# Kernel optimization log

Hardware: AMD Instinct MI355X
Metric: run time of the kernel (lower is better)

The kernel has to match this reference:

```python
import jax, jax.numpy as jnp
import numpy as np

B = 512; LH = 200; N = 40000; F = 256; E = 2000000; EF = 4
K = 8; LP = 50; P = 5000; D = 64; TD = 16; SK = 1000


def _time_enc(t):
    # TimeDualDecayEncoder stand-in: fixed log-spaced frequency cosine features (TGAT-style)
    freqs = 1.0 / (10.0 ** (jnp.arange(TD, dtype=jnp.float32) / TD * 5.0))
    return jnp.cos(t[..., None] * freqs)


def _layernorm(x, g, b):
    m = x.mean(-1, keepdims=True)
    v = ((x - m) ** 2).mean(-1, keepdims=True)
    return (x - m) * jax.lax.rsqrt(v + 1e-5) * g + b


def _gru(x, Wih, Whh, bih, bhh):
    # torch nn.GRU (batch_first), gate order r,z,n; returns final hidden state
    bsz, H = x.shape[0], Whh.shape[1]
    def step(h, xt):
        gi = xt @ Wih.T + bih
        gh = h @ Whh.T + bhh
        ir, iz, inn = jnp.split(gi, 3, -1)
        hr, hz, hn = jnp.split(gh, 3, -1)
        r = jax.nn.sigmoid(ir + hr)
        z = jax.nn.sigmoid(iz + hz)
        n = jnp.tanh(inn + r * hn)
        return (1.0 - z) * n + z * h, None
    h, _ = jax.lax.scan(step, jnp.zeros((bsz, H), x.dtype), jnp.swapaxes(x, 0, 1))
    return h


def _forward(src_node_ids, dst_node_ids, local_neighbor_ids, local_edge_ids, local_times,
             dst_neighbor_ids, dst_edge_ids, dst_times, retrieved_indices,
             node_raw, edge_raw, pool_nodes,
             Wfeat, bfeat, Wedge, bedge, Wtime, btime, Wstruct, bstruct, ln_g, ln_b,
             gruL_Wih, gruL_Whh, gruL_bih, gruL_bhh, gruQ_Wih, gruQ_Whh, gruQ_bih, gruQ_bhh,
             gcn_W, gcn_b, fus_W, fus_b, out_W, out_b):

    def dygkt(nids, eids, times, cur_dst, cur_skill):
        raw = node_raw[nids]                                   # (B,L,F) gather
        nf = raw @ Wfeat.T + bfeat
        ef = edge_raw[eids, 0:1] @ Wedge.T + bedge
        tf = _time_enc(times) @ Wtime.T + btime
        co = (nids == cur_dst[:, None]).astype(jnp.float32)[..., None]
        st = co @ Wstruct.T + bstruct
        sim = (raw[..., 0].astype(jnp.int32) == cur_skill[:, None]).astype(jnp.float32)[..., None]
        sk = sim @ Wstruct.T + bstruct
        return _layernorm(nf + ef + tf + st + sk, ln_g, ln_b)

    def graph_emb(demo):
        # demo: (K,LP) padded node-id sequences (0 = pad). Build dedup'd undirected
        # consecutive-pair graph, run GCNConv (self loops, sym norm), mean-pool.
        ids = demo.reshape(-1)
        M = ids.shape[0]
        valid = ids > 0
        sids = jnp.sort(jnp.where(valid, ids, N))               # invalid -> sentinel N
        uniq = (sids < N) & jnp.concatenate([jnp.ones((1,), bool), sids[1:] != sids[:-1]])
        x = node_raw[jnp.clip(sids, 0, N - 1)] @ Wfeat.T + bfeat
        h = (x @ gcn_W.T) * uniq[:, None]
        u = demo[:, :-1].reshape(-1)
        v = demo[:, 1:].reshape(-1)
        ve = (u > 0) & (v > 0)
        a = jnp.minimum(u, v); b = jnp.maximum(u, v)
        BIG = N * N                                             # fits int32 since N=40000
        skey = jnp.sort(jnp.where(ve, a * N + b, BIG))
        ew = ((skey < BIG) & jnp.concatenate([jnp.ones((1,), bool), skey[1:] != skey[:-1]])).astype(x.dtype)
        su = jnp.clip(jnp.searchsorted(sids, skey // N), 0, M - 1)
        sv = jnp.clip(jnp.searchsorted(sids, skey % N), 0, M - 1)
        uf = uniq.astype(x.dtype)
        deg = jnp.zeros(M, x.dtype).at[su].add(ew).at[sv].add(ew) + uf   # + self loop
        dis = jnp.where(deg > 0, jax.lax.rsqrt(deg), 0.0)
        nrm = (ew * dis[su] * dis[sv])[:, None]
        agg = jnp.zeros_like(h).at[sv].add(nrm * h[su]).at[su].add(nrm * h[sv])
        agg = agg + h * (dis * dis)[:, None] + gcn_b * uf[:, None]
        out = jax.nn.relu(agg)
        return out.sum(0) / jnp.maximum(uniq.sum(), 1).astype(x.dtype)

    dst_skill = node_raw[dst_node_ids, 0].astype(jnp.int32)
    src_skill = node_raw[src_node_ids, 0].astype(jnp.int32)
    local_emb = _gru(dygkt(local_neighbor_ids, local_edge_ids, local_times, dst_node_ids, dst_skill),
                     gruL_Wih, gruL_Whh, gruL_bih, gruL_bhh)
    glob = jax.vmap(graph_emb)(pool_nodes[retrieved_indices])   # (B,D)
    q_emb = _gru(dygkt(dst_neighbor_ids, dst_edge_ids, dst_times, src_node_ids, src_skill),
                 gruQ_Wih, gruQ_Whh, gruQ_bih, gruQ_bhh)
    fused = jax.nn.relu(jnp.concatenate([local_emb, glob], 1) @ fus_W.T + fus_b)
    return fused @ out_W.T + out_b, q_emb @ out_W.T + out_b


def setup_inputs() -> dict:
    key = jax.random.key(0)
    ks = jax.random.split(key, 32)
    f32 = jnp.float32
    node_raw = jax.random.normal(ks[0], (N, F), f32)
    node_raw = node_raw.at[:, 0].set(jax.random.randint(ks[1], (N,), 0, SK).astype(f32))
    edge_raw = jax.random.normal(ks[2], (E, EF), f32)
    ids = jax.random.randint(ks[3], (P, LP), 1, N)
    lens = jax.random.randint(ks[4], (P,), 2, LP + 1)
    pool_nodes = jnp.where(jnp.arange(LP)[None, :] < lens[:, None], ids, 0).astype(jnp.int32)
    def lin(k, o, i, s=0.05):
        kw, kb = jax.random.split(k)
        return jax.random.normal(kw, (o, i), f32) * s, jax.random.normal(kb, (o,), f32) * s
    Wfeat, bfeat = lin(ks[5], D, F)
    Wedge, bedge = lin(ks[6], D, 1)
    Wtime, btime = lin(ks[7], D, TD)
    Wstruct, bstruct = lin(ks[8], D, 1)
    gruL_Wih, gruL_bih = lin(ks[9], 3 * D, D)
    gruL_Whh, gruL_bhh = lin(ks[10], 3 * D, D)
    gruQ_Wih, gruQ_bih = lin(ks[11], 3 * D, D)
    gruQ_Whh, gruQ_bhh = lin(ks[12], 3 * D, D)
    gcn_W, gcn_b = lin(ks[13], D, D)
    fus_W, fus_b = lin(ks[14], D, 2 * D)
    out_W, out_b = lin(ks[15], D, D)
    return dict(
        src_node_ids=jax.random.randint(ks[16], (B,), 0, N).astype(jnp.int32),
        dst_node_ids=jax.random.randint(ks[17], (B,), 0, N).astype(jnp.int32),
        local_neighbor_ids=jax.random.randint(ks[18], (B, LH), 0, N).astype(jnp.int32),
        local_edge_ids=jax.random.randint(ks[19], (B, LH), 0, E).astype(jnp.int32),
        local_times=jax.random.uniform(ks[20], (B, LH), f32) * 100.0,
        dst_neighbor_ids=jax.random.randint(ks[21], (B, LH), 0, N).astype(jnp.int32),
        dst_edge_ids=jax.random.randint(ks[22], (B, LH), 0, E).astype(jnp.int32),
        dst_times=jax.random.uniform(ks[23], (B, LH), f32) * 100.0,
        retrieved_indices=jax.random.randint(ks[24], (B, K), 0, P).astype(jnp.int32),
        node_raw=node_raw, edge_raw=edge_raw, pool_nodes=pool_nodes,
        Wfeat=Wfeat, bfeat=bfeat, Wedge=Wedge, bedge=bedge, Wtime=Wtime, btime=btime,
        Wstruct=Wstruct, bstruct=bstruct, ln_g=jnp.ones((D,), f32), ln_b=jnp.zeros((D,), f32),
        gruL_Wih=gruL_Wih, gruL_Whh=gruL_Whh, gruL_bih=gruL_bih, gruL_bhh=gruL_bhh,
        gruQ_Wih=gruQ_Wih, gruQ_Whh=gruQ_Whh, gruQ_bih=gruQ_bih, gruQ_bhh=gruQ_bhh,
        gcn_W=gcn_W, gcn_b=gcn_b, fus_W=fus_W, fus_b=fus_b, out_W=out_W, out_b=out_b)


def reference(src_node_ids, dst_node_ids, local_neighbor_ids, local_edge_ids, local_times,
              dst_neighbor_ids, dst_edge_ids, dst_times, retrieved_indices,
              node_raw, edge_raw, pool_nodes,
              Wfeat, bfeat, Wedge, bedge, Wtime, btime, Wstruct, bstruct, ln_g, ln_b,
              gruL_Wih, gruL_Whh, gruL_bih, gruL_bhh, gruQ_Wih, gruQ_Whh, gruQ_bih, gruQ_bhh,
              gcn_W, gcn_b, fus_W, fus_b, out_W, out_b):
    return _forward(src_node_ids, dst_node_ids, local_neighbor_ids, local_edge_ids, local_times,
                    dst_neighbor_ids, dst_edge_ids, dst_times, retrieved_indices,
                    node_raw, edge_raw, pool_nodes,
                    Wfeat, bfeat, Wedge, bedge, Wtime, btime, Wstruct, bstruct, ln_g, ln_b,
                    gruL_Wih, gruL_Whh, gruL_bih, gruL_bhh, gruQ_Wih, gruQ_Whh, gruQ_bih, gruQ_bhh,
                    gcn_W, gcn_b, fus_W, fus_b, out_W, out_b)
```

## Files before the change

### kernel.cpp

```cpp
#include <hip/hip_runtime.h>
#include <math.h>

#define NN 40000
#define FF 256
#define DD 64
#define LHH 200
#define BB 512
#define TDD 16
#define GE_HASH 1024

typedef _Float16 h2f __attribute__((ext_vector_type(2)));

__constant__ float TFREQ[16] = {
    1.0f,            0.48696753f,    0.23713737f,    0.115478195f,
    0.056234132f,    0.027384196f,   0.013335215f,   0.0064938162f,
    0.0031622776f,   0.0015399265f,  0.00074989421f, 0.00036517414f,
    0.00017782794f,  8.6596433e-05f, 4.2169650e-05f, 2.0535251e-05f
};

__device__ __forceinline__ float fd2(unsigned a, unsigned b, float c) {
    union { unsigned u; h2f h; } ua, ub;
    ua.u = a; ub.u = b;
    return __builtin_amdgcn_fdot2(ua.h, ub.h, c, false);
}
__device__ __forceinline__ unsigned packrn(float a, float b) {
    union { h2f h; unsigned u; } x;
    x.h.x = (_Float16)a; x.h.y = (_Float16)b;
    return x.u;
}
__device__ __forceinline__ unsigned short f16u(float a) {
    union { _Float16 h; unsigned short u; } x;
    x.h = (_Float16)a;
    return x.u;
}
__device__ __forceinline__ float h16f(unsigned short u) {
    union { unsigned short u; _Float16 h; } x;
    x.u = u;
    return (float)x.h;
}
__device__ __forceinline__ float f16lo(unsigned u) {
    union { unsigned u; h2f h; } x; x.u = u; return (float)x.h.x;
}
__device__ __forceinline__ float f16hi(unsigned u) {
    union { unsigned u; h2f h; } x; x.u = u; return (float)x.h.y;
}
__device__ __forceinline__ unsigned pkrtz_u(float a, float b) {
    auto pk = __builtin_amdgcn_cvt_pkrtz(a, b);
    union { decltype(pk) h; unsigned u; } x;
    x.h = pk;
    return x.u;
}
__device__ __forceinline__ float dpp_xor1(float v) {
    return __int_as_float(
        __builtin_amdgcn_mov_dpp(__float_as_int(v), 0xB1, 0xF, 0xF, true));
}
__device__ __forceinline__ unsigned rlu(unsigned v, int l) {
    return (unsigned)__builtin_amdgcn_readlane((int)v, l);
}
__device__ __forceinline__ float sigm(float x) {
    return __builtin_amdgcn_rcpf(1.f + __expf(-x));
}
__device__ __forceinline__ float tanh_f(float x) {
    float e = __expf(2.f * x);
    return 1.f - 2.f * __builtin_amdgcn_rcpf(e + 1.f);
}
__device__ __forceinline__ int hlookupf(const unsigned* hkey, const int* hslot, unsigned id)
{
    unsigned p = (id * 2654435761u) & (GE_HASH - 1);
    while (hkey[p] != id) p = (p + 1) & (GE_HASH - 1);
    return hslot[p];
}

template<int KDIM>
__global__ void __launch_bounds__(256)
gemm_nt_kernel(const float* __restrict__ A, const float* __restrict__ W,
               const float* __restrict__ bias, float* __restrict__ C, int Nrows)
{
    __shared__ __align__(16) float a_t[128][8];
    __shared__ __align__(16) float wt[8][64];
    const int tid = threadIdx.x;
    const int tx = tid & 15;
    const int ty = tid >> 4;
    const int n0 = blockIdx.x * 128;

    float4 acc[8];
#pragma unroll
    for (int r = 0; r < 8; ++r) acc[r] = make_float4(0.f, 0.f, 0.f, 0.f);

    for (int kc = 0; kc < KDIM; kc += 8) {
        __syncthreads();
        {
            int r = tid >> 1;
            int cc = (tid & 1) * 4;
            int n = n0 + r;
            float4 v = make_float4(0.f, 0.f, 0.f, 0.f);
            if (n < Nrows) v = *(const float4*)(A + (size_t)n * KDIM + kc + cc);
            *(float4*)&a_t[r][cc] = v;
        }
        {
            int m = tid >> 2;
            int f0 = (tid & 3) * 2;
            float2 v = *(const float2*)(W + (size_t)m * KDIM + kc + f0);
            wt[f0][m] = v.x; wt[f0 + 1][m] = v.y;
        }
        __syncthreads();
        float4 w4[8];
#pragma unroll
        for (int f = 0; f < 8; ++f) w4[f] = *(float4*)&wt[f][tx * 4];
#pragma unroll
        for (int rr = 0; rr < 8; ++rr) {
            int row = ty + rr * 16;
            float4 a0 = *(float4*)&a_t[row][0];
            float4 a1 = *(float4*)&a_t[row][4];
            float av[8] = {a0.x, a0.y, a0.z, a0.w, a1.x, a1.y, a1.z, a1.w};
#pragma unroll
            for (int f = 0; f < 8; ++f) {
                acc[rr].x += av[f] * w4[f].x;
                acc[rr].y += av[f] * w4[f].y;
                acc[rr].z += av[f] * w4[f].z;
                acc[rr].w += av[f] * w4[f].w;
            }
        }
    }
    float4 bv = make_float4(0.f, 0.f, 0.f, 0.f);
    if (bias) bv = *(const float4*)(bias + tx * 4);
#pragma unroll
    for (int rr = 0; rr < 8; ++rr) {
        int n = n0 + ty + rr * 16;
        if (n < Nrows) {
            float4 o = acc[rr];
            o.x += bv.x; o.y += bv.y; o.z += bv.z; o.w += bv.w;
            *(float4*)(C + (size_t)n * DD + tx * 4) = o;
        }
    }
}

__global__ void __launch_bounds__(256)
tn_gemm_kernel(const float* __restrict__ proj,
               const float* __restrict__ WihL, const float* __restrict__ WihQ,
               const float* __restrict__ ln_g,
               unsigned short* __restrict__ TnL, unsigned short* __restrict__ TnQ)
{
    const float* Wih = blockIdx.y ? WihQ : WihL;
    unsigned short* Tn = blockIdx.y ? TnQ : TnL;
    __shared__ float wgT[64][193];
    __shared__ __align__(16) float4 at4[64][16];
    const int tid = threadIdx.x;
    const int n0 = blockIdx.x * 64;
    for (int i = tid; i < 192 * 64; i += 256) {
        int j = i >> 6, k = i & 63;
        wgT[k][j] = Wih[i] * ln_g[k];
    }
    for (int i = tid; i < 1024; i += 256) {
        int r = i >> 4, kc = i & 15;
        at4[r][kc] = ((const float4*)(proj + (size_t)(n0 + r) * DD))[kc];
    }
    __syncthreads();
    const int c = tid & 63, wv = tid >> 6;
    float acc0[16], acc1[16], acc2[16];
#pragma unroll
    for (int r = 0; r < 16; ++r) { acc0[r] = 0.f; acc1[r] = 0.f; acc2[r] = 0.f; }
    for (int kc = 0; kc < 16; ++kc) {
        float w0[4], w1[4], w2[4];
#pragma unroll
        for (int q = 0; q < 4; ++q) {
            w0[q] = wgT[kc * 4 + q][c];
            w1[q] = wgT[kc * 4 + q][64 + c];
            w2[q] = wgT[kc * 4 + q][128 + c];
        }
#pragma unroll
        for (int r = 0; r < 16; ++r) {
            float4 a = at4[wv * 16 + r][kc];
            acc0[r] += a.x * w0[0] + a.y * w0[1] + a.z * w0[2] + a.w * w0[3];
            acc1[r] += a.x * w1[0] + a.y * w1[1] + a.z * w1[2] + a.w * w1[3];
            acc2[r] += a.x * w2[0] + a.y * w2[1] + a.z * w2[2] + a.w * w2[3];
        }
    }
#pragma unroll
    for (int r = 0; r < 16; ++r) {
        size_t row = (size_t)(n0 + wv * 16 + r) * 192;
        Tn[row + c]       = f16u(acc0[r]);
        Tn[row + 64 + c]  = f16u(acc1[r]);
        Tn[row + 128 + c] = f16u(acc2[r]);
    }
}

__global__ void __launch_bounds__(192)
consts_kernel(const float* __restrict__ WihL, const float* __restrict__ bihL,
              const float* __restrict__ WhhL, float* __restrict__ outL,
              unsigned* __restrict__ whpL, unsigned* __restrict__ tpkL,
              const float* __restrict__ WihQ, const float* __restrict__ bihQ,
              const float* __restrict__ WhhQ, float* __restrict__ outQ,
              unsigned* __restrict__ whpQ, unsigned* __restrict__ tpkQ,
              unsigned* __restrict__ wtpk,
              const float* __restrict__ ln_g, const float* __restrict__ ln_b,
              const float* __restrict__ Wedge, const float* __restrict__ bedge,
              const float* __restrict__ Wtime, const float* __restrict__ btime,
              const float* __restrict__ Wstruct, const float* __restrict__ bstruct)
{
    const float* Wih = blockIdx.x ? WihQ : WihL;
    const float* bih = blockIdx.x ? bihQ : bihL;
    const float* Whh = blockIdx.x ? WhhQ : WhhL;
    float* out = blockIdx.x ? outQ : outL;
    unsigned* whp = blockIdx.x ? whpQ : whpL;
    unsigned* tpk = blockIdx.x ? tpkQ : tpkL;
    const int j = threadIdx.x;
    float te = 0.f, tw = 0.f, t1 = 0.f, tb0 = 0.f, cc = 0.f;
    float tt[16];
#pragma unroll
    for (int t = 0; t < 16; ++t) tt[t] = 0.f;
    for (int k = 0; k < DD; ++k) {
        float wv = Wih[j * DD + k];
        float wg = wv * ln_g[k];
        te  += wg * Wedge[k];
        tw  += wg * Wstruct[k];
        t1  += wg;
        tb0 += wg * (bedge[k] + btime[k] + 2.f * bstruct[k]);
        cc  += wv * ln_b[k];
#pragma unroll
        for (int t = 0; t < 16; ++t) tt[t] += wg * Wtime[k * TDD + t];
    }
    out[0 * 192 + j] = te;
    out[1 * 192 + j] = tw;
    out[2 * 192 + j] = t1;
    out[3 * 192 + j] = tb0;
    out[4 * 192 + j] = cc + bih[j];
    for (int t = 0; t < 16; ++t) out[(5 + t) * 192 + j] = tt[t];
    for (int q = 0; q < 8; ++q)
        tpk[j * 8 + q] = packrn(tt[2 * q], tt[2 * q + 1]);
    if (blockIdx.x == 0 && j < 64)
        for (int q = 0; q < 8; ++q)
            wtpk[j * 8 + q] = packrn(Wtime[j * TDD + 2 * q], Wtime[j * TDD + 2 * q + 1]);
    for (int k2 = 0; k2 < 32; ++k2)
        whp[j * 32 + k2] = packrn(Whh[j * DD + 2 * k2], Whh[j * DD + 2 * k2 + 1]);
}

struct PS {
    int nid;
    float tn0, tn1, tn2, pv, e0, sk, t;
};

__global__ void __launch_bounds__(256)
pre_kernel(const int* __restrict__ nidsL, const int* __restrict__ eidsL,
           const float* __restrict__ timesL, const int* __restrict__ curL,
           const int* __restrict__ nidsQ, const int* __restrict__ eidsQ,
           const float* __restrict__ timesQ, const int* __restrict__ curQ,
           const float* __restrict__ node_raw, const float* __restrict__ edge_raw,
           const float* __restrict__ proj_node,
           const unsigned short* __restrict__ TnL, const unsigned short* __restrict__ TnQ,
           const float* __restrict__ cstL, const float* __restrict__ cstQ,
           const unsigned* __restrict__ tpkL, const unsigned* __restrict__ tpkQ,
           const unsigned* __restrict__ wtpk,
           const float* __restrict__ bhhL, const float* __restrict__ bhhQ,
           const float* __restrict__ Wedge, const float* __restrict__ bedge,
           const float* __restrict__ Wtime, const float* __restrict__ btime,
           const float* __restrict__ Wstruct, const float* __restrict__ bstruct,
           unsigned* __restrict__ g01out, unsigned short* __restrict__ g2out)
{
    const int tid = threadIdx.x;
    const int d = tid & 63;
    const int seg = blockIdx.x * 4 + (tid >> 6);
    const int blk = seg >> 3, qq = seg & 7;
    const int g = blk >> 9, s = blk & 511;

    const int*            nids  = g ? nidsQ : nidsL;
    const int*            eids  = g ? eidsQ : eidsL;
    const float*          times = g ? timesQ : timesL;
    const int*            curp  = g ? curQ : curL;
    const unsigned short* Tn    = g ? TnQ : TnL;
    const float*          cst   = g ? cstQ : cstL;
    const unsigned*       tpk   = g ? tpkQ : tpkL;
    const float*          bhh   = g ? bhhQ : bhhL;

    unsigned tp0[8], tp1[8], tp2[8], wtp[8];
#pragma unroll
    for (int q4 = 0; q4 < 2; ++q4) {
        uint4 a = *(const uint4*)(tpk + (size_t)(0 * 64 + d) * 8 + 4 * q4);
        tp0[4*q4] = a.x; tp0[4*q4+1] = a.y; tp0[4*q4+2] = a.z; tp0[4*q4+3] = a.w;
        uint4 b = *(const uint4*)(tpk + (size_t)(1 * 64 + d) * 8 + 4 * q4);
        tp1[4*q4] = b.x; tp1[4*q4+1] = b.y; tp1[4*q4+2] = b.z; tp1[4*q4+3] = b.w;
        uint4 c = *(const uint4*)(tpk + (size_t)(2 * 64 + d) * 8 + 4 * q4);
        tp2[4*q4] = c.x; tp2[4*q4+1] = c.y; tp2[4*q4+2] = c.z; tp2[4*q4+3] = c.w;
        uint4 e = *(const uint4*)(wtpk + (size_t)d * 8 + 4 * q4);
        wtp[4*q4] = e.x; wtp[4*q4+1] = e.y; wtp[4*q4+2] = e.z; wtp[4*q4+3] = e.w;
    }
    const float TE0 = cst[0*192 + d], TE1 = cst[0*192 + 64 + d], TE2 = cst[0*192 + 128 + d];
    const float TW0 = cst[1*192 + d], TW1 = cst[1*192 + 64 + d], TW2 = cst[1*192 + 128 + d];
    const float T10 = cst[2*192 + d], T11 = cst[2*192 + 64 + d], T12 = cst[2*192 + 128 + d];
    const float TB0 = cst[3*192 + d], TB1 = cst[3*192 + 64 + d], TB2 = cst[3*192 + 128 + d];
    const float CC0 = cst[4*192 + d] + bhh[d];
    const float CC1 = cst[4*192 + 64 + d] + bhh[64 + d];
    const float CC2 = cst[4*192 + 128 + d];
    const float we_l = Wedge[d];
    const float ws_l = Wstruct[d];
    const float b0_l = bedge[d] + btime[d] + 2.f * bstruct[d];
    const float tfl  = TFREQ[d & 15];

    const int cur = curp[s];
    const int csk = (int)node_raw[(size_t)cur * FF];
    const int* nrow = nids + s * LHH;
    const int* erow = eids + s * LHH;
    const float* trow = times + s * LHH;
    const int lbase = qq * 25;

    auto GATH = [&](PS& P, int i) {
        int l = lbase + i;
        int nid = nrow[l];
        int eid = erow[l];
        P.nid = nid;
        const unsigned short* tb = Tn + (size_t)nid * 192;
        P.tn0 = h16f(tb[d]);
        P.tn1 = h16f(tb[64 + d]);
        P.tn2 = h16f(tb[128 + d]);
        P.pv  = proj_node[(size_t)nid * DD + d];
        P.e0  = edge_raw[(size_t)eid * 4];
        P.sk  = node_raw[(size_t)nid * FF];
        P.t   = trow[l];
    };

    auto EMIT = [&](const PS& P, int i) {
        float cv = __cosf(P.t * tfl);
        float cx = dpp_xor1(cv);
        unsigned cp = pkrtz_u(cv, cx);
        unsigned s0 = rlu(cp, 0),  s1 = rlu(cp, 2),  s2 = rlu(cp, 4),  s3 = rlu(cp, 6);
        unsigned s4 = rlu(cp, 8),  s5 = rlu(cp, 10), s6 = rlu(cp, 12), s7 = rlu(cp, 14);
        float tf = fd2(wtp[7], s7, fd2(wtp[6], s6, fd2(wtp[5], s5, fd2(wtp[4], s4, 0.f))));
        tf = fd2(wtp[3], s3, fd2(wtp[2], s2, fd2(wtp[1], s1, fd2(wtp[0], s0, tf))));
        float flg = ((P.nid == cur) ? 1.f : 0.f) + (((int)P.sk == csk) ? 1.f : 0.f);
        float f = P.pv + P.e0 * we_l + flg * ws_l + b0_l + tf;
        float mu = f;
#pragma unroll
        for (int off = 32; off; off >>= 1) mu += __shfl_xor(mu, off);
        mu *= (1.f / 64.f);
        float dv = f - mu, var = dv * dv;
#pragma unroll
        for (int off = 32; off; off >>= 1) var += __shfl_xor(var, off);
        float rs = rsqrtf(var * (1.f / 64.f) + 1e-5f);
        float c0 = fd2(tp0[7], s7, fd2(tp0[6], s6, fd2(tp0[5], s5, fd2(tp0[4], s4, 0.f))));
        c0 = fd2(tp0[3], s3, fd2(tp0[2], s2, fd2(tp0[1], s1, fd2(tp0[0], s0, c0))));
        float c1 = fd2(tp1[7], s7, fd2(tp1[6], s6, fd2(tp1[5], s5, fd2(tp1[4], s4, 0.f))));
        c1 = fd2(tp1[3], s3, fd2(tp1[2], s2, fd2(tp1[1], s1, fd2(tp1[0], s0, c1))));
        float c2 = fd2(tp2[7], s7, fd2(tp2[6], s6, fd2(tp2[5], s5, fd2(tp2[4], s4, 0.f))));
        c2 = fd2(tp2[3], s3, fd2(tp2[2], s2, fd2(tp2[1], s1, fd2(tp2[0], s0, c2))));
        float g0 = (c0 + P.tn0 + P.e0 * TE0 + flg * TW0 + TB0 - mu * T10) * rs + CC0;
        float g1 = (c1 + P.tn1 + P.e0 * TE1 + flg * TW1 + TB1 - mu * T11) * rs + CC1;
        float g2 = (c2 + P.tn2 + P.e0 * TE2 + flg * TW2 + TB2 - mu * T12) * rs + CC2;
        size_t pos = ((size_t)blk * LHH + (lbase + i)) * 64 + d;
        g01out[pos] = packrn(g0, g1);
        g2out[pos] = f16u(g2);
    };

    PS A, B, C;
    GATH(A, 0);
    GATH(B, 1);
    for (int i = 0; i < 25; ++i) {
        int inext = (i + 2 < 25) ? i + 2 : 24;
        GATH(C, inext);
        EMIT(A, i);
        A = B; B = C;
    }
}

__global__ void __launch_bounds__(64) __attribute__((amdgpu_waves_per_eu(1, 1)))
gru_lite_kernel(const unsigned* __restrict__ g01, const unsigned short* __restrict__ g2a,
                const unsigned* __restrict__ whpL, const unsigned* __restrict__ whpQ,
                const float* __restrict__ bhhL, const float* __restrict__ bhhQ,
                float* __restrict__ embL, float* __restrict__ embQ)
{
    const int blk = blockIdx.x;
    const int g = blk >> 9, s = blk & 511;
    const int d = threadIdx.x;

    const unsigned* whp = g ? whpQ : whpL;
    const float*    bhh = g ? bhhQ : bhhL;
    float*          emb = g ? embQ : embL;

    unsigned w0[32], w1[32], w2[32];
    {
        const unsigned* p0 = whp + (size_t)d * 32;
        const unsigned* p1 = whp + (size_t)(64 + d) * 32;
        const unsigned* p2 = whp + (size_t)(128 + d) * 32;
#pragma unroll
        for (int q4 = 0; q4 < 8; ++q4) {
            uint4 a = *(const uint4*)(p0 + 4 * q4);
            w0[4*q4] = a.x; w0[4*q4+1] = a.y; w0[4*q4+2] = a.z; w0[4*q4+3] = a.w;
            uint4 b = *(const uint4*)(p1 + 4 * q4);
            w1[4*q4] = b.x; w1[4*q4+1] = b.y; w1[4*q4+2] = b.z; w1[4*q4+3] = b.w;
            uint4 c = *(const uint4*)(p2 + 4 * q4);
            w2[4*q4] = c.x; w2[4*q4+1] = c.y; w2[4*q4+2] = c.z; w2[4*q4+3] = c.w;
        }
    }
#pragma unroll
    for (int i = 0; i < 32; ++i) {
        asm volatile("" : "+v"(w0[i]));
        asm volatile("" : "+v"(w1[i]));
        asm volatile("" : "+v"(w2[i]));
    }
    const float BH2 = bhh[128 + d];

    const unsigned* p01 = g01 + (size_t)blk * LHH * 64 + d;
    const unsigned short* p2 = g2a + (size_t)blk * LHH * 64 + d;

    float h = 0.f;

    auto COMPUTE = [&](unsigned pk01, unsigned pk2) {
        float g0 = f16lo(pk01), g1 = f16hi(pk01);
        float g2 = h16f((unsigned short)pk2);
        float hx = dpp_xor1(h);
        unsigned hpu = pkrtz_u(h, hx);
        float a0 = 0.f, a1 = 0.f, a2 = 0.f, e0 = 0.f, e1 = 0.f, e2 = 0.f;
#pragma unroll
        for (int q = 0; q < 32; q += 2) {
            unsigned sa = rlu(hpu, 2 * q);
            unsigned sb = rlu(hpu, 2 * q + 2);
            a0 = fd2(w0[q], sa, a0);
            a1 = fd2(w1[q], sa, a1);
            a2 = fd2(w2[q], sa, a2);
            e0 = fd2(w0[q+1], sb, e0);
            e1 = fd2(w1[q+1], sb, e1);
            e2 = fd2(w2[q+1], sb, e2);
        }
        float mv0 = a0 + e0, mv1 = a1 + e1, mv2 = a2 + e2;
        float r = sigm(g0 + mv0);
        float z = sigm(g1 + mv1);
        float n = tanh_f(g2 + r * (mv2 + BH2));
        h = (1.f - z) * n + z * h;
    };

    unsigned A01[4], A2[4], B01[4], B2[4];
#pragma unroll
    for (int i = 0; i < 4; ++i) {
        A01[i] = p01[(size_t)i * 64];
        A2[i]  = p2[(size_t)i * 64];
    }
    for (int l = 0; l < LHH; l += 8) {
#pragma unroll
        for (int i = 0; i < 4; ++i) {
            int ll = l + 4 + i;
            B01[i] = p01[(size_t)ll * 64];
            B2[i]  = p2[(size_t)ll * 64];
        }
#pragma unroll
        for (int i = 0; i < 4; ++i) COMPUTE(A01[i], A2[i]);
#pragma unroll
        for (int i = 0; i < 4; ++i) {
            int ll = l + 8 + i;
            if (ll > LHH - 1) ll = LHH - 1;
            A01[i] = p01[(size_t)ll * 64];
            A2[i]  = p2[(size_t)ll * 64];
        }
#pragma unroll
        for (int i = 0; i < 4; ++i) COMPUTE(B01[i], B2[i]);
    }
    emb[(size_t)s * DD + d] = h;
}

__global__ void __launch_bounds__(512)
dedup_kernel(const int* __restrict__ retrieved, const int* __restrict__ pool_nodes,
             int* __restrict__ slot_idG, float* __restrict__ disG,
             unsigned* __restrict__ startG, unsigned short* __restrict__ adjG,
             int* __restrict__ Ub)
{
    __shared__ unsigned hkey[GE_HASH];
    __shared__ int hslot[GE_HASH];
    __shared__ unsigned ekey[GE_HASH];
    __shared__ int ids[400];
    __shared__ int slot_id[400];
    __shared__ unsigned deg[400];
    __shared__ float dis[400];
    __shared__ unsigned elist[400];
    __shared__ unsigned scanA[400], scanB[400];
    __shared__ int cursor[400];
    __shared__ unsigned short adjS[800];
    __shared__ int pids[8];
    __shared__ int cntU, cntE;

    const int b = blockIdx.x;
    const int tid = threadIdx.x;

    if (tid < 8) pids[tid] = retrieved[b * 8 + tid];
    if (tid == 0) { cntU = 0; cntE = 0; }
    for (int i = tid; i < GE_HASH; i += 512) { hkey[i] = 0u; ekey[i] = 0u; }
    if (tid < 400) deg[tid] = 0u;
    __syncthreads();

    if (tid < 400) {
        int k = tid / 50, p = tid % 50;
        ids[tid] = pool_nodes[(size_t)pids[k] * 50 + p];
    }
    __syncthreads();

    if (tid < 400) {
        int idi = ids[tid];
        if (idi > 0) {
            unsigned id = (unsigned)idi;
            unsigned p = (id * 2654435761u) & (GE_HASH - 1);
            while (true) {
                unsigned old = atomicCAS(&hkey[p], 0u, id);
                if (old == 0u) {
                    int s = atomicAdd(&cntU, 1);
                    hslot[p] = s; slot_id[s] = idi;
                    break;
                }
                if (old == id) break;
                p = (p + 1) & (GE_HASH - 1);
            }
        }
    }
    __syncthreads();

    if (tid < 8 * 49) {
        int k = tid / 49, p = tid % 49;
        int u = ids[k * 50 + p], v = ids[k * 50 + p + 1];
        if (u > 0 && v > 0) {
            unsigned a = (unsigned)min(u, v), bb = (unsigned)max(u, v);
            unsigned key = a * 40000u + bb;
            unsigned p2 = (key * 2654435761u) & (GE_HASH - 1);
            while (true) {
                unsigned old = atomicCAS(&ekey[p2], 0u, key);
                if (old == 0u) {
                    int su = hlookupf(hkey, hslot, a);
                    int sv = hlookupf(hkey, hslot, bb);
                    int e = atomicAdd(&cntE, 1);
                    elist[e] = ((unsigned)su << 16) | (unsigned)sv;
                    atomicAdd(&deg[su], 1u);
                    atomicAdd(&deg[sv], 1u);
                    break;
                }
                if (old == key) break;
                p2 = (p2 + 1) & (GE_HASH - 1);
            }
        }
    }
    __syncthreads();

    const int U = cntU, EC = cntE;
    if (tid < 400) {
        dis[tid] = rsqrtf((float)deg[tid] + 1.0f);
        scanA[tid] = deg[tid];
    }
    __syncthreads();

    unsigned* src = scanA;
    unsigned* dst = scanB;
    for (int off = 1; off < 400; off <<= 1) {
        if (tid < 400)
            dst[tid] = src[tid] + ((tid >= off) ? src[tid - off] : 0u);
        __syncthreads();
        unsigned* t = src; src = dst; dst = t;
    }
    if (tid < 400) {
        unsigned st = src[tid] - deg[tid];
        cursor[tid] = (int)st;
        if (tid < U) startG[(size_t)b * 404 + tid] = st;
    }
    if (tid == 0) {
        startG[(size_t)b * 404 + U] = (U > 0) ? src[U - 1] : 0u;
        Ub[b] = U;
    }
    __syncthreads();

    if (tid < EC) {
        unsigned pk = elist[tid];
        int su = (int)(pk >> 16), sv = (int)(pk & 0xffffu);
        int pu = atomicAdd(&cursor[su], 1);
        adjS[pu] = (unsigned short)sv;
        int pv = atomicAdd(&cursor[sv], 1);
        adjS[pv] = (unsigned short)su;
    }
    __syncthreads();

    if (tid < 400) {
        slot_idG[(size_t)b * 400 + tid] = (tid < U) ? slot_id[tid] : 0;
        disG[(size_t)b * 400 + tid] = dis[tid];
    }
    for (int i = tid; i < 800; i += 512) {
        unsigned tot = (U > 0) ? src[U - 1] : 0u;
        adjG[(size_t)b * 800 + i] = (i < (int)tot) ? adjS[i] : (unsigned short)0;
    }
}

__global__ void __launch_bounds__(256)
gcn_agg_kernel(const float* __restrict__ hgcn, const float* __restrict__ gcn_b,
               const int* __restrict__ slot_idG, const float* __restrict__ disG,
               const unsigned* __restrict__ startG, const unsigned short* __restrict__ adjG,
               const int* __restrict__ Ub, float* __restrict__ part)
{
    __shared__ int sidS[400];
    __shared__ float disS[400];
    __shared__ unsigned stS[404];
    __shared__ unsigned short adjS[800];
    __shared__ float red[4][64];

    const int b = blockIdx.x, q = blockIdx.y;
    const int tid = threadIdx.x;
    const int lane = tid & 63, w = tid >> 6;
    const int U = Ub[b];

    for (int i = tid; i < 400; i += 256) {
        sidS[i] = slot_idG[(size_t)b * 400 + i];
        disS[i] = disG[(size_t)b * 400 + i];
    }
    for (int i = tid; i < 404; i += 256) stS[i] = startG[(size_t)b * 404 + i];
    for (int i = tid; i < 800; i += 256) adjS[i] = adjG[(size_t)b * 800 + i];
    __syncthreads();

    const float gb = gcn_b[lane];
    float acc = 0.f;

    for (int s = q * 4 + w; s < U; s += 16) {
        int nid = sidS[s];
        float ds = disS[s];
        float v = fmaf(ds * ds, hgcn[(size_t)nid * 64 + lane], gb);
        int a0 = (int)stS[s];
        int cnt = (int)stS[s + 1] - a0;
        for (int e0 = 0; e0 < cnt; e0 += 4) {
            float hv[4], nr[4];
#pragma unroll
            for (int j = 0; j < 4; ++j) {
                int e = e0 + j;
                int ec = (e < cnt) ? e : cnt - 1;
                int o = adjS[a0 + ec];
                nr[j] = (e < cnt) ? ds * disS[o] : 0.f;
                hv[j] = hgcn[(size_t)sidS[o] * 64 + lane];
            }
            v += nr[0] * hv[0] + nr[1] * hv[1] + nr[2] * hv[2] + nr[3] * hv[3];
        }
        acc += fmaxf(v, 0.f);
    }

    red[w][lane] = acc;
    __syncthreads();
    if (tid < 64)
        part[((size_t)b * 4 + q) * 64 + tid] =
            red[0][tid] + red[1][tid] + red[2][tid] + red[3][tid];
}

__global__ void __launch_bounds__(64)
head_kernel(const float* __restrict__ local_emb, const float* __restrict__ part,
            const int* __restrict__ Ub, const float* __restrict__ q_emb,
            const float* __restrict__ fus_W, const float* __restrict__ fus_b,
            const float* __restrict__ out_W, const float* __restrict__ out_b,
            float* __restrict__ out)
{
    __shared__ float cat[128];
    __shared__ float fus[64];
    __shared__ float qv[64];
    const int b = blockIdx.x, d = threadIdx.x;
    cat[d] = local_emb[(size_t)b * 64 + d];
    {
        const float* pb = part + (size_t)b * 4 * 64;
        float gsum = pb[d] + pb[64 + d] + pb[128 + d] + pb[192 + d];
        cat[64 + d] = gsum / (float)max(Ub[b], 1);
    }
    qv[d] = q_emb[(size_t)b * 64 + d];
    __syncthreads();
    float acc = fus_b[d];
    const float* fw = fus_W + (size_t)d * 128;
#pragma unroll 4
    for (int k = 0; k < 128; ++k) acc += cat[k] * fw[k];
    fus[d] = fmaxf(acc, 0.f);
    __syncthreads();
    float o0 = out_b[d], o1 = out_b[d];
    const float* ow = out_W + (size_t)d * 64;
#pragma unroll 4
    for (int k = 0; k < 64; ++k) { float ww = ow[k]; o0 += fus[k] * ww; o1 += qv[k] * ww; }
    out[(size_t)b * 64 + d] = o0;
    out[(size_t)BB * 64 + (size_t)b * 64 + d] = o1;
}

extern "C" void kernel_launch(void* const* d_in, const int* in_sizes, int n_in,
                              void* d_out, int out_size, void* d_ws, size_t ws_size,
                              hipStream_t stream)
{
    const int*   src_ids    = (const int*)d_in[0];
    const int*   dst_ids    = (const int*)d_in[1];
    const int*   l_nids     = (const int*)d_in[2];
    const int*   l_eids     = (const int*)d_in[3];
    const float* l_times    = (const float*)d_in[4];
    const int*   d_nids     = (const int*)d_in[5];
    const int*   d_eids     = (const int*)d_in[6];
    const float* d_times    = (const float*)d_in[7];
    const int*   retr       = (const int*)d_in[8];
    const float* node_raw   = (const float*)d_in[9];
    const float* edge_raw   = (const float*)d_in[10];
    const int*   pool_nodes = (const int*)d_in[11];
    const float* Wfeat  = (const float*)d_in[12];
    const float* bfeat  = (const float*)d_in[13];
    const float* Wedge  = (const float*)d_in[14];
    const float* bedge  = (const float*)d_in[15];
    const float* Wtime  = (const float*)d_in[16];
    const float* btime  = (const float*)d_in[17];
    const float* Wstruct= (const float*)d_in[18];
    const float* bstruct= (const float*)d_in[19];
    const float* ln_g   = (const float*)d_in[20];
    const float* ln_b   = (const float*)d_in[21];
    const float* gruL_Wih = (const float*)d_in[22];
    const float* gruL_Whh = (const float*)d_in[23];
    const float* gruL_bih = (const float*)d_in[24];
    const float* gruL_bhh = (const float*)d_in[25];
    const float* gruQ_Wih = (const float*)d_in[26];
    const float* gruQ_Whh = (const float*)d_in[27];
    const float* gruQ_bih = (const float*)d_in[28];
    const float* gruQ_bhh = (const float*)d_in[29];
    const float* gcn_W  = (const float*)d_in[30];
    const float* gcn_b  = (const float*)d_in[31];
    const float* fus_W  = (const float*)d_in[32];
    const float* fus_b  = (const float*)d_in[33];
    const float* out_W  = (const float*)d_in[34];
    const float* out_b  = (const float*)d_in[35];

    char* wsb = (char*)d_ws;
    auto alloc = [&](size_t bytes) -> void* {
        void* p = (void*)wsb;
        wsb += (bytes + 255) & ~(size_t)255;
        return p;
    };
    float*          proj_node = (float*)alloc((size_t)NN * DD * 4);
    float*          hgcn      = (float*)alloc((size_t)NN * DD * 4);
    unsigned short* TnL16     = (unsigned short*)alloc((size_t)NN * 192 * 2);
    unsigned short* TnQ16     = (unsigned short*)alloc((size_t)NN * 192 * 2);
    float*          cstL      = (float*)alloc(4096 * 4);
    float*          cstQ      = (float*)alloc(4096 * 4);
    unsigned*       whpL      = (unsigned*)alloc(192 * 32 * 4);
    unsigned*       whpQ      = (unsigned*)alloc(192 * 32 * 4);
    unsigned*       tpkL      = (unsigned*)alloc(192 * 8 * 4);
    unsigned*       tpkQ      = (unsigned*)alloc(192 * 8 * 4);
    unsigned*       wtpk      = (unsigned*)alloc(64 * 8 * 4);
    unsigned*       g01       = (unsigned*)alloc((size_t)2 * BB * LHH * 64 * 4);
    unsigned short* g2a       = (unsigned short*)alloc((size_t)2 * BB * LHH * 64 * 2);
    int*            slot_idG  = (int*)alloc((size_t)BB * 400 * 4);
    float*          disG      = (float*)alloc((size_t)BB * 400 * 4);
    unsigned*       startG    = (unsigned*)alloc((size_t)BB * 404 * 4);
    unsigned short* adjG      = (unsigned short*)alloc((size_t)BB * 800 * 2);
    int*            Ubuf      = (int*)alloc((size_t)BB * 4);
    float*          part      = (float*)alloc((size_t)BB * 4 * 64 * 4);
    float*          local_emb = (float*)alloc((size_t)BB * DD * 4);
    float*          q_emb     = (float*)alloc((size_t)BB * DD * 4);

    dim3 g1((NN + 127) / 128);
    gemm_nt_kernel<FF><<<g1, 256, 0, stream>>>(node_raw, Wfeat, bfeat, proj_node, NN);

    consts_kernel<<<2, 192, 0, stream>>>(gruL_Wih, gruL_bih, gruL_Whh, cstL, whpL, tpkL,
                                         gruQ_Wih, gruQ_bih, gruQ_Whh, cstQ, whpQ, tpkQ,
                                         wtpk, ln_g, ln_b, Wedge, bedge, Wtime, btime,
                                         Wstruct, bstruct);

    tn_gemm_kernel<<<dim3(NN / 64, 2), 256, 0, stream>>>(proj_node, gruL_Wih, gruQ_Wih,
                                                         ln_g, TnL16, TnQ16);

    dedup_kernel<<<BB, 512, 0, stream>>>(retr, pool_nodes, slot_idG, disG,
                                         startG, adjG, Ubuf);

    pre_kernel<<<2 * BB * 2, 256, 0, stream>>>(
        l_nids, l_eids, l_times, dst_ids,
        d_nids, d_eids, d_times, src_ids,
        node_raw, edge_raw, proj_node, TnL16, TnQ16, cstL, cstQ,
        tpkL, tpkQ, wtpk, gruL_bhh, gruQ_bhh,
        Wedge, bedge, Wtime, btime, Wstruct, bstruct,
        g01, g2a);

    gemm_nt_kernel<DD><<<g1, 256, 0, stream>>>(proj_node, gcn_W, nullptr, hgcn, NN);

    gru_lite_kernel<<<2 * BB, 64, 0, stream>>>(
        g01, g2a, whpL, whpQ, gruL_bhh, gruQ_bhh, local_emb, q_emb);

    gcn_agg_kernel<<<dim3(BB, 4), 256, 0, stream>>>(
        hgcn, gcn_b, slot_idG, disG, startG, adjG, Ubuf, part);

    head_kernel<<<BB, 64, 0, stream>>>(local_emb, part, Ubuf, q_emb,
        fus_W, fus_b, out_W, out_b, (float*)d_out);
}
```

Before: 294.9 us.

## Compact gathered node/edge scalars and projections to fp16 before pre_kernel

Adds a compaction kernel that pulls the skill scalar out of node_raw and edge feature 0 out of edge_raw into dense fp16/u16 arrays. tn_gemm also writes an fp16 copy of proj_node. pre_kernel then gathers from these narrow arrays instead of doing strided fp32 row gathers, which cuts scattered memory traffic. The cost is a full strided pass over the 2M-edge table (about 32MB read) every call, plus fp16 rounding of the projection and edge features, and skill values truncated to 16 bits.

```diff
diff --git a/kernel.cpp b/kernel.cpp
--- a/kernel.cpp
+++ b/kernel.cpp
@@ -7,6 +7,7 @@
 #define LHH 200
 #define BB 512
 #define TDD 16
+#define EE 2000000
 #define GE_HASH 1024
 
 typedef _Float16 h2f __attribute__((ext_vector_type(2)));
@@ -69,6 +70,18 @@
     unsigned p = (id * 2654435761u) & (GE_HASH - 1);
     while (hkey[p] != id) p = (p + 1) & (GE_HASH - 1);
     return hslot[p];
+}
+
+__global__ void __launch_bounds__(256)
+compact_kernel(const float* __restrict__ node_raw, const float* __restrict__ edge_raw,
+               unsigned short* __restrict__ skill16, unsigned short* __restrict__ e016)
+{
+    const int stride = gridDim.x * 256;
+    int i = blockIdx.x * 256 + threadIdx.x;
+    for (int n = i; n < NN; n += stride)
+        skill16[n] = (unsigned short)(int)node_raw[(size_t)n * FF];
+    for (int e = i; e < EE; e += stride)
+        e016[e] = f16u(edge_raw[(size_t)e * 4]);
 }
 
 template<int KDIM>
@@ -139,7 +152,8 @@
 tn_gemm_kernel(const float* __restrict__ proj,
                const float* __restrict__ WihL, const float* __restrict__ WihQ,
                const float* __restrict__ ln_g,
-               unsigned short* __restrict__ TnL, unsigned short* __restrict__ TnQ)
+               unsigned short* __restrict__ TnL, unsigned short* __restrict__ TnQ,
+               unsigned short* __restrict__ proj16)
 {
     const float* Wih = blockIdx.y ? WihQ : WihL;
     unsigned short* Tn = blockIdx.y ? TnQ : TnL;
@@ -156,6 +170,11 @@
         at4[r][kc] = ((const float4*)(proj + (size_t)(n0 + r) * DD))[kc];
     }
     __syncthreads();
+    if (blockIdx.y == 0) {
+        const float* atf = (const float*)at4;
+        for (int i = tid; i < 64 * 64; i += 256)
+            proj16[(size_t)(n0 + (i >> 6)) * DD + (i & 63)] = f16u(atf[i]);
+    }
     const int c = tid & 63, wv = tid >> 6;
     float acc0[16], acc1[16], acc2[16];
 #pragma unroll
@@ -236,8 +255,8 @@
 }
 
 struct PS {
-    int nid;
-    float tn0, tn1, tn2, pv, e0, sk, t;
+    int nid, skI;
+    float tn0, tn1, tn2, pv, e0, t;
 };
 
 __global__ void __launch_bounds__(256)
@@ -245,8 +264,8 @@
            const float* __restrict__ timesL, const int* __restrict__ curL,
            const int* __restrict__ nidsQ, const int* __restrict__ eidsQ,
            const float* __restrict__ timesQ, const int* __restrict__ curQ,
-           const float* __restrict__ node_raw, const float* __restrict__ edge_raw,
-           const float* __restrict__ proj_node,
+           const unsigned short* __restrict__ skill16, const unsigned short* __restrict__ e016,
+           const unsigned short* __restrict__ proj16,
            const unsigned short* __restrict__ TnL, const unsigned short* __restrict__ TnQ,
            const float* __restrict__ cstL, const float* __restrict__ cstQ,
            const unsigned* __restrict__ tpkL, const unsigned* __restrict__ tpkQ,
@@ -297,7 +316,7 @@
     const float tfl  = TFREQ[d & 15];
 
     const int cur = curp[s];
-    const int csk = (int)node_raw[(size_t)cur * FF];
+    const int csk = (int)skill16[cur];
     const int* nrow = nids + s * LHH;
     const int* erow = eids + s * LHH;
     const float* trow = times + s * LHH;
@@ -312,9 +331,9 @@
         P.tn0 = h16f(tb[d]);
         P.tn1 = h16f(tb[64 + d]);
         P.tn2 = h16f(tb[128 + d]);
-        P.pv  = proj_node[(size_t)nid * DD + d];
-        P.e0  = edge_raw[(size_t)eid * 4];
-        P.sk  = node_raw[(size_t)nid * FF];
+        P.pv  = h16f(proj16[(size_t)nid * DD + d]);
+        P.e0  = h16f(e016[eid]);
+        P.skI = (int)skill16[nid];
         P.t   = trow[l];
     };
 
@@ -326,7 +345,7 @@
         unsigned s4 = rlu(cp, 8),  s5 = rlu(cp, 10), s6 = rlu(cp, 12), s7 = rlu(cp, 14);
         float tf = fd2(wtp[7], s7, fd2(wtp[6], s6, fd2(wtp[5], s5, fd2(wtp[4], s4, 0.f))));
         tf = fd2(wtp[3], s3, fd2(wtp[2], s2, fd2(wtp[1], s1, fd2(wtp[0], s0, tf))));
-        float flg = ((P.nid == cur) ? 1.f : 0.f) + (((int)P.sk == csk) ? 1.f : 0.f);
+        float flg = ((P.nid == cur) ? 1.f : 0.f) + ((P.skI == csk) ? 1.f : 0.f);
         float f = P.pv + P.e0 * we_l + flg * ws_l + b0_l + tf;
         float mu = f;
 #pragma unroll
@@ -720,6 +739,9 @@
     float*          hgcn      = (float*)alloc((size_t)NN * DD * 4);
     unsigned short* TnL16     = (unsigned short*)alloc((size_t)NN * 192 * 2);
     unsigned short* TnQ16     = (unsigned short*)alloc((size_t)NN * 192 * 2);
+    unsigned short* proj16    = (unsigned short*)alloc((size_t)NN * DD * 2);
+    unsigned short* skill16   = (unsigned short*)alloc((size_t)NN * 2);
+    unsigned short* e016      = (unsigned short*)alloc((size_t)EE * 2);
     float*          cstL      = (float*)alloc(4096 * 4);
     float*          cstQ      = (float*)alloc(4096 * 4);
     unsigned*       whpL      = (unsigned*)alloc(192 * 32 * 4);
@@ -741,13 +763,15 @@
     dim3 g1((NN + 127) / 128);
     gemm_nt_kernel<FF><<<g1, 256, 0, stream>>>(node_raw, Wfeat, bfeat, proj_node, NN);
 
+    compact_kernel<<<2048, 256, 0, stream>>>(node_raw, edge_raw, skill16, e016);
+
     consts_kernel<<<2, 192, 0, stream>>>(gruL_Wih, gruL_bih, gruL_Whh, cstL, whpL, tpkL,
                                          gruQ_Wih, gruQ_bih, gruQ_Whh, cstQ, whpQ, tpkQ,
                                          wtpk, ln_g, ln_b, Wedge, bedge, Wtime, btime,
                                          Wstruct, bstruct);
 
     tn_gemm_kernel<<<dim3(NN / 64, 2), 256, 0, stream>>>(proj_node, gruL_Wih, gruQ_Wih,
-                                                         ln_g, TnL16, TnQ16);
+                                                         ln_g, TnL16, TnQ16, proj16);
 
     dedup_kernel<<<BB, 512, 0, stream>>>(retr, pool_nodes, slot_idG, disG,
                                          startG, adjG, Ubuf);
@@ -755,7 +779,7 @@
     pre_kernel<<<2 * BB * 2, 256, 0, stream>>>(
         l_nids, l_eids, l_times, dst_ids,
         d_nids, d_eids, d_times, src_ids,
-        node_raw, edge_raw, proj_node, TnL16, TnQ16, cstL, cstQ,
+        skill16, e016, proj16, TnL16, TnQ16, cstL, cstQ,
         tpkL, tpkQ, wtpk, gruL_bhh, gruQ_bhh,
         Wedge, bedge, Wtime, btime, Wstruct, bstruct,
         g01, g2a);
```

Result: slower. 302.9 us (+2.7%).
